# Performance work log

Measured on AMD Instinct MI355X. Metric: run time of the kernel, lower is better.

## Reference

```python
import jax, jax.numpy as jnp
import numpy as np

B, DIM, N = 4, 256, 2048
HEADS, DIM_HEAD = 8, 64
HIDDEN = HEADS * DIM_HEAD
SCALE = DIM_HEAD ** -0.5


def setup_inputs() -> dict:
    key = jax.random.key(0)
    k0, k1, k2, k3 = jax.random.split(key, 4)
    x = jax.random.normal(k0, (B, DIM, N), dtype=jnp.float32)
    # Conv1d kernel-size-1 weights == plain matrices over channels
    w_qkv = jax.random.normal(k1, (3 * HIDDEN, DIM), dtype=jnp.float32) * (DIM ** -0.5)
    w_out = jax.random.normal(k2, (DIM, HIDDEN), dtype=jnp.float32) * (HIDDEN ** -0.5)
    b_out = jax.random.normal(k3, (DIM,), dtype=jnp.float32) * 0.01
    return {"x": x, "w_qkv": w_qkv, "w_out": w_out, "b_out": b_out}


def reference(x, w_qkv, w_out, b_out):
    b, c, n = x.shape
    # 1x1 conv projection: [3H, C] x [b, C, n] -> [b, 3H, n]
    qkv = jnp.einsum('oc,bcn->bon', w_qkv, x)
    q, k, v = jnp.split(qkv, 3, axis=1)
    # [b, heads, dim_head, n]
    q = q.reshape(b, HEADS, DIM_HEAD, n) * SCALE
    k = k.reshape(b, HEADS, DIM_HEAD, n)
    v = v.reshape(b, HEADS, DIM_HEAD, n)
    sim = jnp.einsum('bhcn,bhcm->bhnm', q, k)          # [b,h,n,n]
    attn = jax.nn.softmax(sim, axis=-1)
    out = jnp.einsum('bhnm,bhcm->bhcn', attn, v)       # [b,h,dh,n]
    out = out.reshape(b, HIDDEN, n)
    return jnp.einsum('oc,bcn->bon', w_out, out) + b_out[None, :, None]
```

## Files before the change

kernel.cpp:

```cpp
#include <hip/hip_runtime.h>
#include <math.h>

#define BB 4
#define CDIM 256
#define NN 2048
#define HEADS 8
#define DH 64
#define HIDDEN 512
#define THREEH 1536
#define QSCALE 0.18033688011112042f

typedef __attribute__((ext_vector_type(8))) short bf16x8;
typedef __attribute__((ext_vector_type(4))) float f32x4;

static __device__ inline unsigned short f2bf(float f) {
    unsigned u = __float_as_uint(f);
    u += 0x7fff + ((u >> 16) & 1);
    return (unsigned short)(u >> 16);
}
#if __has_builtin(__builtin_amdgcn_cvt_pk_bf16_f32)
static __device__ inline unsigned pk2(float a, float b) {
    auto v = __builtin_amdgcn_cvt_pk_bf16_f32(a, b);
    return __builtin_bit_cast(unsigned, v);
}
#else
static __device__ inline unsigned pk2(float a, float b) {
    return (unsigned)f2bf(a) | ((unsigned)f2bf(b) << 16);
}
#endif
#if __has_builtin(__builtin_amdgcn_exp2f)
#define EXP2(x) __builtin_amdgcn_exp2f(x)
#else
#define EXP2(x) exp2f(x)
#endif
#define MFMA16(a, b, c) __builtin_amdgcn_mfma_f32_16x16x32_bf16(a, b, c, 0, 0, 0)
#define SWZC(row, ch) ((((ch) ^ ((row) & 7)) << 3))

__global__ __launch_bounds__(256) void prep_all(const float* __restrict__ x,
                                                const float* __restrict__ wqkv,
                                                const float* __restrict__ wout,
                                                unsigned short* __restrict__ Xt,
                                                unsigned* __restrict__ Wqb,
                                                unsigned* __restrict__ Wob) {
    __shared__ float Ls[64][65];
    const int bx = blockIdx.x;
    if (bx < 512) {
        const int n0 = (bx & 31) * 64, c0 = ((bx >> 5) & 3) * 64, b = bx >> 7;
        const int t = threadIdx.x;
        const int r16 = t >> 4, c16 = t & 15;
#pragma unroll
        for (int s = 0; s < 4; ++s) {
            const int c = s * 16 + r16;
            float4 v = *(const float4*)&x[((size_t)(b * CDIM + c0 + c)) * NN + n0 + c16 * 4];
            *(float4*)&Ls[c][c16 * 4] = v;
        }
        __syncthreads();
#pragma unroll
        for (int s = 0; s < 4; ++s) {
            const int n = s * 16 + r16;
            const int c4 = c16 * 4;
            uint2 u;
            u.x = pk2(Ls[c4][n], Ls[c4 + 1][n]);
            u.y = pk2(Ls[c4 + 2][n], Ls[c4 + 3][n]);
            *(uint2*)&Xt[((size_t)(b * NN) + n0 + n) * CDIM + c0 + c4] = u;
        }
    } else if (bx < 536) {
        const int tt = (bx - 512) * 256 + threadIdx.x;
#pragma unroll 4
        for (int j = 0; j < 16; ++j) {
            const int i4 = tt + j * 6144;
            const int e = i4 * 4;
            const float s = ((e >> 8) < HIDDEN) ? QSCALE : 1.f;
            float4 v = *(const float4*)&wqkv[e];
            Wqb[i4 * 2 + 0] = pk2(v.x * s, v.y * s);
            Wqb[i4 * 2 + 1] = pk2(v.z * s, v.w * s);
        }
    } else {
        const int tt = (bx - 536) * 256 + threadIdx.x;
#pragma unroll 4
        for (int j = 0; j < 16; ++j) {
            const int i4 = tt + j * 2048;
            const int e = i4 * 4;
            float4 v = *(const float4*)&wout[e];
            Wob[i4 * 2 + 0] = pk2(v.x, v.y);
            Wob[i4 * 2 + 1] = pk2(v.z, v.w);
        }
    }
}

__global__ __launch_bounds__(256, 3) void qkv_gemm(const unsigned short* __restrict__ Xt,
                                                   const unsigned short* __restrict__ Wqb,
                                                   unsigned short* __restrict__ Qb,
                                                   unsigned short* __restrict__ Kb,
                                                   unsigned short* __restrict__ Vb) {
    __shared__ unsigned short Xs[128 * 64], Ws[128 * 64];
    const int bn0 = blockIdx.x * 128, o0 = blockIdx.y * 128;
    const int t = threadIdx.x, l = t & 63, w = t >> 6, lo = l & 15, quad = l >> 4;
    const int wo = (w >> 1) * 64, wn = (w & 1) * 64;
    const int sr = t >> 1, scb = (t & 1) * 4;
    const bool isV = (o0 >= 2 * HIDDEN);
    f32x4 acc[4][4];
#pragma unroll
    for (int i = 0; i < 4; ++i)
#pragma unroll
        for (int j = 0; j < 4; ++j) acc[i][j] = (f32x4){0.f, 0.f, 0.f, 0.f};

    for (int kc = 0; kc < CDIM; kc += 64) {
        __syncthreads();
#pragma unroll
        for (int j = 0; j < 4; ++j) {
            const int ch = scb + j;
            *(uint4*)&Xs[sr * 64 + SWZC(sr, ch)] =
                *(const uint4*)&Xt[(size_t)(bn0 + sr) * CDIM + kc + ch * 8];
            *(uint4*)&Ws[sr * 64 + SWZC(sr, ch)] =
                *(const uint4*)&Wqb[(size_t)(o0 + sr) * CDIM + kc + ch * 8];
        }
        __syncthreads();
#pragma unroll
        for (int kk = 0; kk < 2; ++kk) {
            const int swz = SWZC(lo, kk * 4 + quad);
            if (!isV) {
                bf16x8 af[4], bv[4];
#pragma unroll
                for (int ot = 0; ot < 4; ++ot) af[ot] = *(const bf16x8*)&Ws[(wo + ot * 16 + lo) * 64 + swz];
#pragma unroll
                for (int nt = 0; nt < 4; ++nt) bv[nt] = *(const bf16x8*)&Xs[(wn + nt * 16 + lo) * 64 + swz];
#pragma unroll
                for (int ot = 0; ot < 4; ++ot)
#pragma unroll
                    for (int nt = 0; nt < 4; ++nt) acc[ot][nt] = MFMA16(af[ot], bv[nt], acc[ot][nt]);
            } else {
                bf16x8 af[4], bv[4];
#pragma unroll
                for (int mt = 0; mt < 4; ++mt) af[mt] = *(const bf16x8*)&Xs[(wn + mt * 16 + lo) * 64 + swz];
#pragma unroll
                for (int ot = 0; ot < 4; ++ot) bv[ot] = *(const bf16x8*)&Ws[(wo + ot * 16 + lo) * 64 + swz];
#pragma unroll
                for (int mt = 0; mt < 4; ++mt)
#pragma unroll
                    for (int ot = 0; ot < 4; ++ot) acc[mt][ot] = MFMA16(af[mt], bv[ot], acc[mt][ot]);
            }
        }
    }
    if (!isV) {
#pragma unroll
        for (int ot = 0; ot < 4; ++ot) {
            const int og = o0 + wo + ot * 16 + quad * 4;
            const int h = (og >> 6) & 7;
            const int c0 = og & 63;
            unsigned short* dst = (og >= HIDDEN) ? Kb : Qb;
#pragma unroll
            for (int nt = 0; nt < 4; ++nt) {
                const int bn = bn0 + wn + nt * 16 + lo;
                const int b = bn >> 11, n = bn & 2047;
                uint2 u;
                u.x = pk2(acc[ot][nt][0], acc[ot][nt][1]);
                u.y = pk2(acc[ot][nt][2], acc[ot][nt][3]);
                *(uint2*)&dst[(((size_t)(b * HEADS + h)) * NN + n) * DH + c0] = u;
            }
        }
    } else {
#pragma unroll
        for (int mt = 0; mt < 4; ++mt) {
            const int bn = bn0 + wn + mt * 16 + quad * 4;
            const int b = bn >> 11, m = bn & 2047;
#pragma unroll
            for (int ot = 0; ot < 4; ++ot) {
                const int og = o0 + wo + ot * 16 + lo;
                const int h = (og >> 6) & 7;
                const int c = og & 63;
                uint2 u;
                u.x = pk2(acc[mt][ot][0], acc[mt][ot][1]);
                u.y = pk2(acc[mt][ot][2], acc[mt][ot][3]);
                *(uint2*)&Vb[(((size_t)(b * HEADS + h)) * DH + c) * NN + m] = u;
            }
        }
    }
}

__global__ __launch_bounds__(256, 4) void flash_attn(const unsigned short* __restrict__ Qb,
                                                     const unsigned short* __restrict__ Kb,
                                                     const unsigned short* __restrict__ Vb,
                                                     unsigned short* __restrict__ Yb) {
    __shared__ unsigned short Ks[64 * 64], Vs[64 * 64], Ps[128 * 64];
    const int flat = blockIdx.x;
    const int rest = flat >> 3;
    const int bh = ((rest & 3) << 3) | (flat & 7);
    const int q0 = (rest >> 2) * 128;
    const int b = bh >> 3, h = bh & 7;
    const int t = threadIdx.x, l = t & 63, w = t >> 6, lo = l & 15, quad = l >> 4;
    const unsigned short* Qp = Qb + (size_t)bh * NN * DH;
    const unsigned short* Kp = Kb + (size_t)bh * NN * DH;
    const unsigned short* Vp = Vb + (size_t)bh * DH * NN;
    const int qbase = q0 + 32 * w;
    bf16x8 bQ[2][2];
#pragma unroll
    for (int qt = 0; qt < 2; ++qt)
#pragma unroll
        for (int hh = 0; hh < 2; ++hh)
            bQ[qt][hh] = *(const bf16x8*)&Qp[(size_t)(qbase + qt * 16 + lo) * DH + hh * 32 + quad * 8];
    f32x4 O[4][2], lacc[2];
#pragma unroll
    for (int i = 0; i < 4; ++i)
#pragma unroll
        for (int j = 0; j < 2; ++j) O[i][j] = (f32x4){0.f, 0.f, 0.f, 0.f};
#pragma unroll
    for (int j = 0; j < 2; ++j) lacc[j] = (f32x4){0.f, 0.f, 0.f, 0.f};
    const int sr = t >> 3, sc = t & 7;
    const int kst0 = sr * 64 + SWZC(sr, sc);
    const int key = lo & 7;
    bf16x8 aOnes;
    {
        const short v = (lo == 0) ? (short)0x3F80 : (short)0;
        aOnes = (bf16x8){v, v, v, v, v, v, v, v};
    }
    uint4 rk0 = *(const uint4*)&Kp[(size_t)sr * DH + sc * 8];
    uint4 rk1 = *(const uint4*)&Kp[(size_t)(sr + 32) * DH + sc * 8];
    uint4 rv0 = *(const uint4*)&Vp[(size_t)sr * NN + sc * 8];
    uint4 rv1 = *(const uint4*)&Vp[(size_t)(sr + 32) * NN + sc * 8];

#pragma unroll 1
    for (int m0 = 0; m0 < NN; m0 += 64) {
        __syncthreads();
        *(uint4*)&Ks[kst0] = rk0;
        *(uint4*)&Ks[kst0 + 2048] = rk1;
        *(uint4*)&Vs[kst0] = rv0;
        *(uint4*)&Vs[kst0 + 2048] = rv1;
        __syncthreads();
        {
            const int m1 = (m0 + 64 < NN) ? (m0 + 64) : m0;
            rk0 = *(const uint4*)&Kp[(size_t)(m1 + sr) * DH + sc * 8];
            rk1 = *(const uint4*)&Kp[(size_t)(m1 + sr + 32) * DH + sc * 8];
            rv0 = *(const uint4*)&Vp[(size_t)sr * NN + m1 + sc * 8];
            rv1 = *(const uint4*)&Vp[(size_t)(sr + 32) * NN + m1 + sc * 8];
        }
#pragma unroll
        for (int nt = 0; nt < 4; ++nt) {
            const int rb = (nt * 16 + lo) * 64;
            bf16x8 a0 = *(const bf16x8*)&Ks[rb + SWZC(lo, quad)];
            bf16x8 a1 = *(const bf16x8*)&Ks[rb + SWZC(lo, quad + 4)];
            const int pcol = (((nt * 2 + (quad >> 1)) ^ key) << 3) + (quad & 1) * 4;
#pragma unroll
            for (int qt = 0; qt < 2; ++qt) {
                f32x4 z = (f32x4){0.f, 0.f, 0.f, 0.f};
                z = MFMA16(a0, bQ[qt][0], z);
                z = MFMA16(a1, bQ[qt][1], z);
                f32x4 p;
#pragma unroll
                for (int i = 0; i < 4; ++i) p[i] = EXP2(z[i]);
                uint2 u;
                u.x = pk2(p[0], p[1]);
                u.y = pk2(p[2], p[3]);
                *(uint2*)&Ps[(32 * w + qt * 16 + lo) * 64 + pcol] = u;
            }
        }
        asm volatile("s_waitcnt lgkmcnt(0)" ::: "memory");
        bf16x8 pb[2][2];
#pragma unroll
        for (int qt = 0; qt < 2; ++qt) {
            const int prow = (32 * w + qt * 16 + lo) * 64;
            pb[qt][0] = *(const bf16x8*)&Ps[prow + SWZC(lo, quad)];
            pb[qt][1] = *(const bf16x8*)&Ps[prow + SWZC(lo, quad + 4)];
        }
#pragma unroll
        for (int ct = 0; ct < 4; ++ct) {
            const int rb = (ct * 16 + lo) * 64;
            bf16x8 a0 = *(const bf16x8*)&Vs[rb + SWZC(lo, quad)];
            bf16x8 a1 = *(const bf16x8*)&Vs[rb + SWZC(lo, quad + 4)];
#pragma unroll
            for (int qt = 0; qt < 2; ++qt) {
                O[ct][qt] = MFMA16(a0, pb[qt][0], O[ct][qt]);
                O[ct][qt] = MFMA16(a1, pb[qt][1], O[ct][qt]);
            }
        }
#pragma unroll
        for (int qt = 0; qt < 2; ++qt) {
            lacc[qt] = MFMA16(aOnes, pb[qt][0], lacc[qt]);
            lacc[qt] = MFMA16(aOnes, pb[qt][1], lacc[qt]);
        }
    }
#pragma unroll
    for (int qt = 0; qt < 2; ++qt) {
        const float lv = __shfl(lacc[qt][0], lo);
        const float inv = 1.f / lv;
        const int q = qbase + qt * 16 + lo;
        unsigned short* yrow = Yb + ((size_t)(b * NN) + q) * HIDDEN + h * DH;
#pragma unroll
        for (int ct = 0; ct < 4; ++ct) {
            uint2 u;
            u.x = pk2(O[ct][qt][0] * inv, O[ct][qt][1] * inv);
            u.y = pk2(O[ct][qt][2] * inv, O[ct][qt][3] * inv);
            *(uint2*)&yrow[ct * 16 + quad * 4] = u;
        }
    }
}

__global__ __launch_bounds__(256, 4) void out_gemm(const unsigned short* __restrict__ Yb,
                                                   const unsigned short* __restrict__ Wob,
                                                   const float* __restrict__ bias,
                                                   float* __restrict__ out) {
    __shared__ unsigned short Ys[128 * 64], Wos[64 * 64];
    const int bn0 = blockIdx.x * 128, o0 = blockIdx.y * 64;
    const int t = threadIdx.x, l = t & 63, w = t >> 6, lo = l & 15, quad = l >> 4;
    const int wn = w * 32;
    const int sr = t >> 1, scb = (t & 1) * 4;
    const int sr2 = t >> 2, scb2 = (t & 3) * 2;
    f32x4 acc[2][4];
#pragma unroll
    for (int i = 0; i < 2; ++i)
#pragma unroll
        for (int j = 0; j < 4; ++j) acc[i][j] = (f32x4){0.f, 0.f, 0.f, 0.f};

    for (int kc = 0; kc < HIDDEN; kc += 64) {
        __syncthreads();
#pragma unroll
        for (int j = 0; j < 4; ++j) {
            const int ch = scb + j;
            *(uint4*)&Ys[sr * 64 + SWZC(sr, ch)] =
                *(const uint4*)&Yb[(size_t)(bn0 + sr) * HIDDEN + kc + ch * 8];
        }
#pragma unroll
        for (int j = 0; j < 2; ++j) {
            const int ch = scb2 + j;
            *(uint4*)&Wos[sr2 * 64 + SWZC(sr2, ch)] =
                *(const uint4*)&Wob[(size_t)(o0 + sr2) * HIDDEN + kc + ch * 8];
        }
        __syncthreads();
#pragma unroll
        for (int kk = 0; kk < 2; ++kk) {
            const int swz = SWZC(lo, kk * 4 + quad);
            bf16x8 bv[4];
#pragma unroll
            for (int ot = 0; ot < 4; ++ot) bv[ot] = *(const bf16x8*)&Wos[(ot * 16 + lo) * 64 + swz];
#pragma unroll
            for (int mt = 0; mt < 2; ++mt) {
                bf16x8 av = *(const bf16x8*)&Ys[(wn + mt * 16 + lo) * 64 + swz];
#pragma unroll
                for (int ot = 0; ot < 4; ++ot) acc[mt][ot] = MFMA16(av, bv[ot], acc[mt][ot]);
            }
        }
    }
#pragma unroll
    for (int mt = 0; mt < 2; ++mt) {
        const int bn = bn0 + wn + mt * 16 + quad * 4;
        const int b = bn >> 11, n = bn & 2047;
#pragma unroll
        for (int ot = 0; ot < 4; ++ot) {
            const int o = o0 + ot * 16 + lo;
            *(f32x4*)&out[((size_t)(b * CDIM + o)) * NN + n] = acc[mt][ot] + bias[o];
        }
    }
}

extern "C" void kernel_launch(void* const* d_in, const int* in_sizes, int n_in,
                              void* d_out, int out_size, void* d_ws, size_t ws_size,
                              hipStream_t stream) {
    const float* x     = (const float*)d_in[0];
    const float* w_qkv = (const float*)d_in[1];
    const float* w_out = (const float*)d_in[2];
    const float* b_out = (const float*)d_in[3];
    float* out = (float*)d_out;

    unsigned short* Wqb = (unsigned short*)d_ws;
    unsigned short* Wob = Wqb + (size_t)THREEH * CDIM;
    unsigned short* Xt  = Wob + (size_t)CDIM * HIDDEN;
    unsigned short* Qb  = Xt + (size_t)BB * NN * CDIM;
    unsigned short* Kb  = Qb + (size_t)BB * HEADS * NN * DH;
    unsigned short* Vb  = Kb + (size_t)BB * HEADS * NN * DH;
    unsigned short* Yb  = Vb + (size_t)BB * HEADS * DH * NN;

    prep_all<<<544, 256, 0, stream>>>(x, w_qkv, w_out, Xt, (unsigned*)Wqb, (unsigned*)Wob);
    qkv_gemm<<<dim3(BB * NN / 128, THREEH / 128), 256, 0, stream>>>(Xt, Wqb, Qb, Kb, Vb);
    flash_attn<<<512, 256, 0, stream>>>(Qb, Kb, Vb, Yb);
    out_gemm<<<dim3(BB * NN / 128, CDIM / 64), 256, 0, stream>>>(Yb, Wob, b_out, out);
}
```

Before: 148.9 us.

## Split attention KV range across two blocks and combine partial sums

Splits the key/value sequence in half so the attention kernel launches twice as many blocks, each writing unnormalized fp32 partial outputs and row sums. A new combine kernel adds the two halves, normalizes, and writes the bf16 hidden tensor. This aims to raise GPU occupancy and parallelism, at the cost of extra global memory traffic for the fp32 partials and an additional kernel launch.

After: 153.0 us. +2.7%, slower.

```diff
diff --git a/kernel.cpp b/kernel.cpp
--- a/kernel.cpp
+++ b/kernel.cpp
@@ -181,17 +181,20 @@
 __global__ __launch_bounds__(256, 4) void flash_attn(const unsigned short* __restrict__ Qb,
                                                      const unsigned short* __restrict__ Kb,
                                                      const unsigned short* __restrict__ Vb,
-                                                     unsigned short* __restrict__ Yb) {
+                                                     float* __restrict__ Op,
+                                                     float* __restrict__ lp) {
     __shared__ unsigned short Ks[64 * 64], Vs[64 * 64], Ps[128 * 64];
     const int flat = blockIdx.x;
-    const int rest = flat >> 3;
-    const int bh = ((rest & 3) << 3) | (flat & 7);
+    const int sp = flat >> 9;
+    const int f2 = flat & 511;
+    const int rest = f2 >> 3;
+    const int bh = ((rest & 3) << 3) | (f2 & 7);
     const int q0 = (rest >> 2) * 128;
-    const int b = bh >> 3, h = bh & 7;
     const int t = threadIdx.x, l = t & 63, w = t >> 6, lo = l & 15, quad = l >> 4;
     const unsigned short* Qp = Qb + (size_t)bh * NN * DH;
     const unsigned short* Kp = Kb + (size_t)bh * NN * DH;
     const unsigned short* Vp = Vb + (size_t)bh * DH * NN;
+    const int kv0 = sp * (NN / 2), kvEnd = kv0 + NN / 2;
     const int qbase = q0 + 32 * w;
     bf16x8 bQ[2][2];
 #pragma unroll
@@ -214,13 +217,13 @@
         const short v = (lo == 0) ? (short)0x3F80 : (short)0;
         aOnes = (bf16x8){v, v, v, v, v, v, v, v};
     }
-    uint4 rk0 = *(const uint4*)&Kp[(size_t)sr * DH + sc * 8];
-    uint4 rk1 = *(const uint4*)&Kp[(size_t)(sr + 32) * DH + sc * 8];
-    uint4 rv0 = *(const uint4*)&Vp[(size_t)sr * NN + sc * 8];
-    uint4 rv1 = *(const uint4*)&Vp[(size_t)(sr + 32) * NN + sc * 8];
+    uint4 rk0 = *(const uint4*)&Kp[(size_t)(kv0 + sr) * DH + sc * 8];
+    uint4 rk1 = *(const uint4*)&Kp[(size_t)(kv0 + sr + 32) * DH + sc * 8];
+    uint4 rv0 = *(const uint4*)&Vp[(size_t)sr * NN + kv0 + sc * 8];
+    uint4 rv1 = *(const uint4*)&Vp[(size_t)(sr + 32) * NN + kv0 + sc * 8];
 
 #pragma unroll 1
-    for (int m0 = 0; m0 < NN; m0 += 64) {
+    for (int m0 = kv0; m0 < kvEnd; m0 += 64) {
         __syncthreads();
         *(uint4*)&Ks[kst0] = rk0;
         *(uint4*)&Ks[kst0 + 2048] = rk1;
@@ -228,7 +231,7 @@
         *(uint4*)&Vs[kst0 + 2048] = rv1;
         __syncthreads();
         {
-            const int m1 = (m0 + 64 < NN) ? (m0 + 64) : m0;
+            const int m1 = (m0 + 64 < kvEnd) ? (m0 + 64) : m0;
             rk0 = *(const uint4*)&Kp[(size_t)(m1 + sr) * DH + sc * 8];
             rk1 = *(const uint4*)&Kp[(size_t)(m1 + sr + 32) * DH + sc * 8];
             rv0 = *(const uint4*)&Vp[(size_t)sr * NN + m1 + sc * 8];
@@ -281,18 +284,33 @@
     }
 #pragma unroll
     for (int qt = 0; qt < 2; ++qt) {
-        const float lv = __shfl(lacc[qt][0], lo);
-        const float inv = 1.f / lv;
         const int q = qbase + qt * 16 + lo;
-        unsigned short* yrow = Yb + ((size_t)(b * NN) + q) * HIDDEN + h * DH;
+        float* orow = Op + ((size_t)(sp * 32 + bh) * NN + q) * DH;
 #pragma unroll
         for (int ct = 0; ct < 4; ++ct) {
-            uint2 u;
-            u.x = pk2(O[ct][qt][0] * inv, O[ct][qt][1] * inv);
-            u.y = pk2(O[ct][qt][2] * inv, O[ct][qt][3] * inv);
-            *(uint2*)&yrow[ct * 16 + quad * 4] = u;
-        }
-    }
+            *(f32x4*)&orow[ct * 16 + quad * 4] = O[ct][qt];
+        }
+        if (quad == 0) lp[(size_t)(sp * 32 + bh) * NN + q] = lacc[qt][0];
+    }
+}
+
+__global__ __launch_bounds__(256) void combine(const float* __restrict__ Op,
+                                               const float* __restrict__ lp,
+                                               unsigned short* __restrict__ Yb) {
+    const int t = blockIdx.x * 256 + threadIdx.x;
+    const int c4 = (t & 15) * 4;
+    const int q = (t >> 4) & (NN - 1);
+    const int bh = t >> 15;
+    const size_t half = (size_t)32 * NN * DH;
+    const size_t base = ((size_t)bh * NN + q) * DH + c4;
+    f32x4 o0 = *(const f32x4*)&Op[base];
+    f32x4 o1 = *(const f32x4*)&Op[base + half];
+    const float inv = 1.f / (lp[(size_t)bh * NN + q] + lp[(size_t)32 * NN + (size_t)bh * NN + q]);
+    uint2 u;
+    u.x = pk2((o0[0] + o1[0]) * inv, (o0[1] + o1[1]) * inv);
+    u.y = pk2((o0[2] + o1[2]) * inv, (o0[3] + o1[3]) * inv);
+    const int b = bh >> 3, h = bh & 7;
+    *(uint2*)&Yb[((size_t)(b * NN + q)) * HIDDEN + h * DH + c4] = u;
 }
 
 __global__ __launch_bounds__(256, 4) void out_gemm(const unsigned short* __restrict__ Yb,
@@ -368,9 +386,12 @@
     unsigned short* Kb  = Qb + (size_t)BB * HEADS * NN * DH;
     unsigned short* Vb  = Kb + (size_t)BB * HEADS * NN * DH;
     unsigned short* Yb  = Vb + (size_t)BB * HEADS * DH * NN;
+    float* Op = (float*)(Yb + (size_t)BB * NN * HIDDEN);
+    float* lp = Op + (size_t)2 * BB * HEADS * NN * DH;
 
     prep_all<<<544, 256, 0, stream>>>(x, w_qkv, w_out, Xt, (unsigned*)Wqb, (unsigned*)Wob);
     qkv_gemm<<<dim3(BB * NN / 128, THREEH / 128), 256, 0, stream>>>(Xt, Wqb, Qb, Kb, Vb);
-    flash_attn<<<512, 256, 0, stream>>>(Qb, Kb, Vb, Yb);
+    flash_attn<<<1024, 256, 0, stream>>>(Qb, Kb, Vb, Op, lp);
+    combine<<<(BB * HEADS * NN * 16) / 256, 256, 0, stream>>>(Op, lp, Yb);
     out_gemm<<<dim3(BB * NN / 128, CDIM / 64), 256, 0, stream>>>(Yb, Wob, b_out, out);
 }
```

## Redistribute softmax probabilities via permlane swaps instead of LDS round-trip

Applied to the files above, without the earlier changes.

The exponentiated score tile is no longer written to a shared-memory P buffer and read back in the B-operand layout. Instead, each wave packs the bf16 values in registers and uses v_permlane32_swap and v_permlane16_swap to move them into the layout the PV MFMA expects. This removes LDS traffic, the lgkmcnt wait and the P shared buffer, which lowers LDS use per block. It also adds s_setprio around the PV MFMAs. The lane permutation must match the MFMA operand layout exactly or the results will be wrong.

After: 148.4 us. Within noise of the previous version (-0.3%).

```diff
diff --git a/kernel.cpp b/kernel.cpp
--- a/kernel.cpp
+++ b/kernel.cpp
@@ -12,6 +12,7 @@
 
 typedef __attribute__((ext_vector_type(8))) short bf16x8;
 typedef __attribute__((ext_vector_type(4))) float f32x4;
+typedef __attribute__((ext_vector_type(4))) unsigned uint4v;
 
 static __device__ inline unsigned short f2bf(float f) {
     unsigned u = __float_as_uint(f);
@@ -35,6 +36,13 @@
 #endif
 #define MFMA16(a, b, c) __builtin_amdgcn_mfma_f32_16x16x32_bf16(a, b, c, 0, 0, 0)
 #define SWZC(row, ch) ((((ch) ^ ((row) & 7)) << 3))
+
+static __device__ inline void swap16(unsigned &a, unsigned &b) {
+    asm("v_permlane16_swap_b32 %0, %1" : "+v"(a), "+v"(b));
+}
+static __device__ inline void swap32(unsigned &a, unsigned &b) {
+    asm("v_permlane32_swap_b32 %0, %1" : "+v"(a), "+v"(b));
+}
 
 __global__ __launch_bounds__(256) void prep_all(const float* __restrict__ x,
                                                 const float* __restrict__ wqkv,
@@ -182,7 +190,7 @@
                                                      const unsigned short* __restrict__ Kb,
                                                      const unsigned short* __restrict__ Vb,
                                                      unsigned short* __restrict__ Yb) {
-    __shared__ unsigned short Ks[64 * 64], Vs[64 * 64], Ps[128 * 64];
+    __shared__ unsigned short Ks[64 * 64], Vs[64 * 64];
     const int flat = blockIdx.x;
     const int rest = flat >> 3;
     const int bh = ((rest & 3) << 3) | (flat & 7);
@@ -206,14 +214,13 @@
         for (int j = 0; j < 2; ++j) O[i][j] = (f32x4){0.f, 0.f, 0.f, 0.f};
 #pragma unroll
     for (int j = 0; j < 2; ++j) lacc[j] = (f32x4){0.f, 0.f, 0.f, 0.f};
-    const int sr = t >> 3, sc = t & 7;
-    const int kst0 = sr * 64 + SWZC(sr, sc);
-    const int key = lo & 7;
     bf16x8 aOnes;
     {
         const short v = (lo == 0) ? (short)0x3F80 : (short)0;
         aOnes = (bf16x8){v, v, v, v, v, v, v, v};
     }
+    const int sr = t >> 3, sc = t & 7;
+    const int kst0 = sr * 64 + SWZC(sr, sc);
     uint4 rk0 = *(const uint4*)&Kp[(size_t)sr * DH + sc * 8];
     uint4 rk1 = *(const uint4*)&Kp[(size_t)(sr + 32) * DH + sc * 8];
     uint4 rv0 = *(const uint4*)&Vp[(size_t)sr * NN + sc * 8];
@@ -234,44 +241,47 @@
             rv0 = *(const uint4*)&Vp[(size_t)sr * NN + m1 + sc * 8];
             rv1 = *(const uint4*)&Vp[(size_t)(sr + 32) * NN + m1 + sc * 8];
         }
+        unsigned wv[2][4][2];
 #pragma unroll
         for (int nt = 0; nt < 4; ++nt) {
             const int rb = (nt * 16 + lo) * 64;
             bf16x8 a0 = *(const bf16x8*)&Ks[rb + SWZC(lo, quad)];
             bf16x8 a1 = *(const bf16x8*)&Ks[rb + SWZC(lo, quad + 4)];
-            const int pcol = (((nt * 2 + (quad >> 1)) ^ key) << 3) + (quad & 1) * 4;
 #pragma unroll
             for (int qt = 0; qt < 2; ++qt) {
                 f32x4 z = (f32x4){0.f, 0.f, 0.f, 0.f};
                 z = MFMA16(a0, bQ[qt][0], z);
                 z = MFMA16(a1, bQ[qt][1], z);
-                f32x4 p;
-#pragma unroll
-                for (int i = 0; i < 4; ++i) p[i] = EXP2(z[i]);
-                uint2 u;
-                u.x = pk2(p[0], p[1]);
-                u.y = pk2(p[2], p[3]);
-                *(uint2*)&Ps[(32 * w + qt * 16 + lo) * 64 + pcol] = u;
-            }
-        }
-        asm volatile("s_waitcnt lgkmcnt(0)" ::: "memory");
+                wv[qt][nt][0] = pk2(EXP2(z[0]), EXP2(z[1]));
+                wv[qt][nt][1] = pk2(EXP2(z[2]), EXP2(z[3]));
+            }
+        }
         bf16x8 pb[2][2];
 #pragma unroll
         for (int qt = 0; qt < 2; ++qt) {
-            const int prow = (32 * w + qt * 16 + lo) * 64;
-            pb[qt][0] = *(const bf16x8*)&Ps[prow + SWZC(lo, quad)];
-            pb[qt][1] = *(const bf16x8*)&Ps[prow + SWZC(lo, quad + 4)];
+#pragma unroll
+            for (int f = 0; f < 2; ++f) {
+                unsigned x0 = wv[qt][2 * f][0], y0 = wv[qt][2 * f + 1][0];
+                unsigned x1 = wv[qt][2 * f][1], y1 = wv[qt][2 * f + 1][1];
+                swap32(x0, y0); swap16(x0, y0);
+                swap32(x1, y1); swap16(x1, y1);
+                uint4v uu;
+                uu.x = x0; uu.y = x1; uu.z = y0; uu.w = y1;
+                pb[qt][f] = __builtin_bit_cast(bf16x8, uu);
+            }
         }
 #pragma unroll
         for (int ct = 0; ct < 4; ++ct) {
             const int rb = (ct * 16 + lo) * 64;
             bf16x8 a0 = *(const bf16x8*)&Vs[rb + SWZC(lo, quad)];
             bf16x8 a1 = *(const bf16x8*)&Vs[rb + SWZC(lo, quad + 4)];
+            __builtin_amdgcn_s_setprio(1);
 #pragma unroll
             for (int qt = 0; qt < 2; ++qt) {
                 O[ct][qt] = MFMA16(a0, pb[qt][0], O[ct][qt]);
                 O[ct][qt] = MFMA16(a1, pb[qt][1], O[ct][qt]);
             }
+            __builtin_amdgcn_s_setprio(0);
         }
 #pragma unroll
         for (int qt = 0; qt < 2; ++qt) {
```
